# Performance work log

Measured on AMD Instinct MI355X. Metric: run time of the kernel, lower is better.

## Reference

```python
import jax, jax.numpy as jnp
import numpy as np

N = 50000   # nodes
E = 800000  # edges (avg degree 16)
C = 96      # in = hidden = out channels


def setup_inputs() -> dict:
    key = jax.random.key(0)
    ks = jax.random.split(key, 8)
    s = np.float32(1.0 / np.sqrt(C))
    x = jax.random.normal(ks[0], (N, C), dtype=jnp.float32)
    edge_index = jax.random.randint(ks[1], (2, E), 0, N, dtype=jnp.int64)
    W1 = jax.random.normal(ks[2], (C, C), dtype=jnp.float32) * s
    Wr1 = jax.random.normal(ks[3], (C, C), dtype=jnp.float32) * s
    b1 = jnp.zeros((C,), dtype=jnp.float32)
    W2 = jax.random.normal(ks[4], (C, C), dtype=jnp.float32) * s
    Wr2 = jax.random.normal(ks[5], (C, C), dtype=jnp.float32) * s
    b2 = jnp.zeros((C,), dtype=jnp.float32)
    return {"x": x, "edge_index": edge_index,
            "W1": W1, "Wr1": Wr1, "b1": b1,
            "W2": W2, "Wr2": Wr2, "b2": b2}


def spline_conv(x, edge_index, W, W_root, b):
    """Gather-transform-scatter message passing (SplineConv core, mean aggr)."""
    src, dst = edge_index[0], edge_index[1]
    h = x @ W                                   # [N, C] transform once per node
    msg = h[src]                                # [E, C] edge gather
    agg = jax.ops.segment_sum(msg, dst, num_segments=N)        # scatter-add
    deg = jax.ops.segment_sum(jnp.ones((E,), x.dtype), dst, num_segments=N)
    agg = agg / jnp.maximum(deg, 1.0)[:, None]  # mean aggregation
    return agg + x @ W_root + b                 # root weight + bias


def reference(x, edge_index, W1, Wr1, b1, W2, Wr2, b2):
    h = jax.nn.relu(spline_conv(x, edge_index, W1, Wr1, b1))
    out = spline_conv(h, edge_index, W2, Wr2, b2)
    return out.reshape(-1)  # generalization of x.view(1600)
```

## Files before the change

### kernel.cpp

```cpp
#include <hip/hip_runtime.h>

#define C 96
#define BKT_SHIFT 9
#define BKT_SIZE 512
#define CAP 10240
#define EB 2048
typedef unsigned short u16;
typedef unsigned int u32;
typedef __attribute__((ext_vector_type(8))) short short8;
typedef __attribute__((ext_vector_type(4))) float floatx4;

__device__ inline u16 f2bf(float f) {
    union { float f; u32 u; } v; v.f = f;
    u32 r = v.u + 0x7fff + ((v.u >> 16) & 1);
    return (u16)(r >> 16);
}

__global__ __launch_bounds__(256) void prep_kernel(const float* __restrict__ x,
                                                   u16* __restrict__ xb, int n16, int CX,
                                                   const float* W0, const float* W1,
                                                   const float* W2, const float* W3,
                                                   u16* T0, u16* T1, u16* T2, u16* T3,
                                                   int* __restrict__ bkt_cnt) {
    int bid = blockIdx.x;
    int t = threadIdx.x;
    if (bid < CX) {
        int i = bid * 256 + t;
        if (i >= n16) return;
        const float4* p = (const float4*)x + (size_t)i * 4;
        float4 a = p[0], b = p[1], c = p[2], d = p[3];
        short8 o0, o1;
        o0[0] = (short)f2bf(a.x); o0[1] = (short)f2bf(a.y);
        o0[2] = (short)f2bf(a.z); o0[3] = (short)f2bf(a.w);
        o0[4] = (short)f2bf(b.x); o0[5] = (short)f2bf(b.y);
        o0[6] = (short)f2bf(b.z); o0[7] = (short)f2bf(b.w);
        o1[0] = (short)f2bf(c.x); o1[1] = (short)f2bf(c.y);
        o1[2] = (short)f2bf(c.z); o1[3] = (short)f2bf(c.w);
        o1[4] = (short)f2bf(d.x); o1[5] = (short)f2bf(d.y);
        o1[6] = (short)f2bf(d.z); o1[7] = (short)f2bf(d.w);
        *(short8*)(xb + (size_t)i * 16) = o0;
        *(short8*)(xb + (size_t)i * 16 + 8) = o1;
    } else if (bid < CX + 4) {
        int w = bid - CX;
        const float* W = w == 0 ? W0 : w == 1 ? W1 : w == 2 ? W2 : W3;
        u16* T = w == 0 ? T0 : w == 1 ? T1 : w == 2 ? T2 : T3;
        for (int i = t; i < C * C; i += 256) {
            int k = i / C, n = i - k * C;
            T[n * C + k] = f2bf(W[i]);
        }
    } else {
        if (t < 128) bkt_cnt[t] = 0;
    }
}

__global__ __launch_bounds__(256) void binA_kernel(const int* __restrict__ src,
                                                   const int* __restrict__ dst,
                                                   int* __restrict__ bkt_cnt,
                                                   u32* __restrict__ stage, int E) {
    __shared__ u32 s_word[EB];
    __shared__ u32 s_addr[EB];
    __shared__ int s_cnt[128];
    __shared__ int s_inc[128];
    __shared__ int s_base[128];
    int t = threadIdx.x;
    int e0 = blockIdx.x * EB;
    int cnt_here = min(EB, E - e0);

    for (int i = t; i < 128; i += 256) s_cnt[i] = 0;
    __syncthreads();

    int my_src[EB / 256], my_dl[EB / 256], my_b[EB / 256], my_rank[EB / 256];
    int nmine = 0;
#pragma unroll
    for (int k = 0; k < EB / 256; k++) {
        int i = t + k * 256;
        if (i < cnt_here) {
            int s = src[e0 + i], d = dst[e0 + i];
            int b = d >> BKT_SHIFT;
            my_src[nmine] = s;
            my_dl[nmine] = d & (BKT_SIZE - 1);
            my_b[nmine] = b;
            my_rank[nmine] = atomicAdd(&s_cnt[b], 1);
            nmine++;
        }
    }
    __syncthreads();

    if (t < 128) s_inc[t] = s_cnt[t];
    __syncthreads();
    for (int off = 1; off < 128; off <<= 1) {
        int x = (t >= off && t < 128) ? s_inc[t - off] : 0;
        __syncthreads();
        if (t < 128) s_inc[t] += x;
        __syncthreads();
    }

    if (t < 128 && s_cnt[t] > 0)
        s_base[t] = t * CAP + atomicAdd(&bkt_cnt[t], s_cnt[t]);
    __syncthreads();

    for (int k = 0; k < nmine; k++) {
        int b = my_b[k];
        int slot = (s_inc[b] - s_cnt[b]) + my_rank[k];
        s_word[slot] = ((u32)my_dl[k] << 16) | (u32)my_src[k];
        s_addr[slot] = (u32)(s_base[b] + my_rank[k]);
    }
    __syncthreads();

    for (int i = t; i < cnt_here; i += 256) stage[s_addr[i]] = s_word[i];
}

__global__ __launch_bounds__(256) void binB_kernel(const u32* __restrict__ stage,
                                                   const int* __restrict__ bkt_cnt,
                                                   int* __restrict__ deg,
                                                   int* __restrict__ row_off,
                                                   u16* __restrict__ csr, int N) {
    __shared__ int cnt[BKT_SIZE];
    __shared__ int cur[BKT_SIZE];
    __shared__ int ssum[256];
    int b = blockIdx.x;
    int n0 = b << BKT_SHIFT;
    int nn = min(BKT_SIZE, N - n0);
    int t = threadIdx.x;
    int s0 = b * CAP;
    int s1 = s0 + bkt_cnt[b];

    for (int i = t; i < BKT_SIZE; i += 256) cnt[i] = 0;
    __syncthreads();

    for (int i = s0 + t; i < s1; i += 256) atomicAdd(&cnt[stage[i] >> 16], 1);
    __syncthreads();

    int a0 = cnt[2 * t], a1 = cnt[2 * t + 1];
    ssum[t] = a0 + a1;
    __syncthreads();
    for (int off = 1; off < 256; off <<= 1) {
        int x = (t >= off) ? ssum[t - off] : 0;
        __syncthreads();
        ssum[t] += x;
        __syncthreads();
    }
    int excl = ssum[t] - (a0 + a1);
    cur[2 * t] = s0 + excl;
    cur[2 * t + 1] = s0 + excl + a0;
    if (2 * t < nn) { deg[n0 + 2 * t] = a0; row_off[n0 + 2 * t] = s0 + excl; }
    if (2 * t + 1 < nn) { deg[n0 + 2 * t + 1] = a1; row_off[n0 + 2 * t + 1] = s0 + excl + a0; }
    __syncthreads();

    for (int i = s0 + t; i < s1; i += 256) {
        u32 w = stage[i];
        int p = atomicAdd(&cur[w >> 16], 1);
        csr[p] = (u16)(w & 0xffffu);
    }
}

template <bool RELU, typename OT>
__global__ __launch_bounds__(256, 4) void layer_kernel(const u16* __restrict__ X,
                                                       const int* __restrict__ row_off,
                                                       const int* __restrict__ deg,
                                                       const u16* __restrict__ csr,
                                                       const u16* __restrict__ WTA,
                                                       const u16* __restrict__ WTR,
                                                       const float* __restrict__ BIAS,
                                                       OT* __restrict__ Y, int n) {
    __shared__ u16 sA[64 * 104];
    const int t = threadIdx.x;
    const int row0 = blockIdx.x * 64;

    {
        int nl = t >> 2;
        int node = row0 + nl;
        int q = t & 3;
        float acc[24];
#pragma unroll
        for (int i = 0; i < 24; i++) acc[i] = 0.f;
        int d = 0;
        if (node < n) {
            int start = row_off[node];
            d = deg[node];
            const u16* Xq = X + q * 24;
            int j = 0;
            for (; j + 4 <= d; j += 4) {
                int si[4];
#pragma unroll
                for (int k = 0; k < 4; k++) si[k] = csr[start + j + k];
                uint4 v[4][3];
#pragma unroll
                for (int k = 0; k < 4; k++) {
                    const u16* p = Xq + (size_t)si[k] * C;
                    v[k][0] = *(const uint4*)(p);
                    v[k][1] = *(const uint4*)(p + 8);
                    v[k][2] = *(const uint4*)(p + 16);
                }
#pragma unroll
                for (int k = 0; k < 4; k++)
#pragma unroll
                    for (int c = 0; c < 3; c++) {
                        u32 ww[4] = {v[k][c].x, v[k][c].y, v[k][c].z, v[k][c].w};
#pragma unroll
                        for (int i = 0; i < 4; i++) {
                            union { u32 u; float f; } a0, b0;
                            a0.u = ww[i] << 16; b0.u = ww[i] & 0xffff0000u;
                            acc[c * 8 + 2 * i]     += a0.f;
                            acc[c * 8 + 2 * i + 1] += b0.f;
                        }
                    }
            }
            for (; j < d; j++) {
                const u16* p = Xq + (size_t)csr[start + j] * C;
                uint4 v0 = *(const uint4*)(p);
                uint4 v1 = *(const uint4*)(p + 8);
                uint4 v2 = *(const uint4*)(p + 16);
                uint4 vv[3] = {v0, v1, v2};
#pragma unroll
                for (int c = 0; c < 3; c++) {
                    u32 ww[4] = {vv[c].x, vv[c].y, vv[c].z, vv[c].w};
#pragma unroll
                    for (int i = 0; i < 4; i++) {
                        union { u32 u; float f; } a0, b0;
                        a0.u = ww[i] << 16; b0.u = ww[i] & 0xffff0000u;
                        acc[c * 8 + 2 * i]     += a0.f;
                        acc[c * 8 + 2 * i + 1] += b0.f;
                    }
                }
            }
        }
        float inv = 1.0f / fmaxf((float)d, 1.0f);
        u16* dl = sA + nl * 104 + q * 24;
#pragma unroll
        for (int c = 0; c < 3; c++) {
            short8 o;
#pragma unroll
            for (int i = 0; i < 8; i++) o[i] = (short)f2bf(acc[c * 8 + i] * inv);
            *(short8*)(dl + c * 8) = o;
        }
    }
    __syncthreads();

    const int lane = t & 63;
    const int w = t >> 6;
    const int quad = lane >> 4;
    const int l16 = lane & 15;
    const int r0 = row0 + w * 16;

    floatx4 acc6[6];
#pragma unroll
    for (int i = 0; i < 6; i++) acc6[i] = (floatx4){0.f, 0.f, 0.f, 0.f};

    {
        const u16* Ap = sA + (w * 16 + l16) * 104 + quad * 8;
        const u16* Wp = WTA + l16 * C + quad * 8;
#pragma unroll
        for (int ks = 0; ks < 3; ks++) {
            short8 a = *(const short8*)(Ap + ks * 32);
#pragma unroll
            for (int nt = 0; nt < 6; nt++) {
                short8 b = *(const short8*)(Wp + nt * 16 * C + ks * 32);
                acc6[nt] = __builtin_amdgcn_mfma_f32_16x16x32_bf16(a, b, acc6[nt], 0, 0, 0);
            }
        }
    }
    {
        int arow = r0 + l16;
        if (arow >= n) arow = n - 1;
        const u16* Xp = X + (size_t)arow * C + quad * 8;
        const u16* Wp = WTR + l16 * C + quad * 8;
#pragma unroll
        for (int ks = 0; ks < 3; ks++) {
            short8 a = *(const short8*)(Xp + ks * 32);
#pragma unroll
            for (int nt = 0; nt < 6; nt++) {
                short8 b = *(const short8*)(Wp + nt * 16 * C + ks * 32);
                acc6[nt] = __builtin_amdgcn_mfma_f32_16x16x32_bf16(a, b, acc6[nt], 0, 0, 0);
            }
        }
    }

#pragma unroll
    for (int nt = 0; nt < 6; nt++) {
        int cc = nt * 16 + l16;
        float bv = BIAS[cc];
#pragma unroll
        for (int r = 0; r < 4; r++) {
            int row = r0 + quad * 4 + r;
            if (row >= n) continue;
            float v = acc6[nt][r] + bv;
            if (RELU) v = fmaxf(v, 0.f);
            if constexpr (sizeof(OT) == 2) Y[(size_t)row * C + cc] = (OT)f2bf(v);
            else                           Y[(size_t)row * C + cc] = (OT)v;
        }
    }
}

extern "C" void kernel_launch(void* const* d_in, const int* in_sizes, int n_in,
                              void* d_out, int out_size, void* d_ws, size_t ws_size,
                              hipStream_t stream) {
    const float* x   = (const float*)d_in[0];
    const int*   ei  = (const int*)d_in[1];
    const float* W1  = (const float*)d_in[2];
    const float* Wr1 = (const float*)d_in[3];
    const float* b1  = (const float*)d_in[4];
    const float* W2  = (const float*)d_in[5];
    const float* Wr2 = (const float*)d_in[6];
    const float* b2  = (const float*)d_in[7];
    float* out = (float*)d_out;

    const int N = in_sizes[0] / C;
    const int E = in_sizes[1] / 2;
    const int* src = ei;
    const int* dst = ei + E;

    const int nbkt = (N + BKT_SIZE - 1) >> BKT_SHIFT;
    int Npad = (N + 63) & ~63;

    int*   bkt_cnt = (int*)d_ws;
    int*   deg     = bkt_cnt + 128;
    int*   row_off = deg + Npad;
    u32*   stage   = (u32*)(row_off + Npad);
    u16*   csr     = (u16*)(stage + (size_t)nbkt * CAP);
    u16*   xb      = csr + (((size_t)nbkt * CAP + 7) & ~(size_t)7);
    u16*   h1b     = xb + (size_t)N * C;
    u16*   wt      = h1b + (size_t)N * C;
    u16 *wt1 = wt, *wtr1 = wt + C * C, *wt2 = wt + 2 * C * C, *wtr2 = wt + 3 * C * C;

    const int grid64 = (N + 63) / 64;
    const int n16    = N * C / 16;
    const int CX     = (n16 + 255) / 256;
    const int DB     = (E + EB - 1) / EB;

    prep_kernel<<<CX + 5, 256, 0, stream>>>(x, xb, n16, CX,
                                            W1, Wr1, W2, Wr2, wt1, wtr1, wt2, wtr2,
                                            bkt_cnt);
    binA_kernel<<<DB, 256, 0, stream>>>(src, dst, bkt_cnt, stage, E);
    binB_kernel<<<nbkt, 256, 0, stream>>>(stage, bkt_cnt, deg, row_off, csr, N);

    layer_kernel<true, u16><<<grid64, 256, 0, stream>>>(xb, row_off, deg, csr,
                                                        wt1, wtr1, b1, h1b, N);
    layer_kernel<false, float><<<grid64, 256, 0, stream>>>(h1b, row_off, deg, csr,
                                                           wt2, wtr2, b2, out, N);
}
```

Before: 201.6 us.

## Merge prep work into binning kernel and sort rows by degree within blocks

Folds the x-to-bf16 conversion and weight transposition into the edge-binning kernel as extra blocks, leaving a tiny kernel that only zeroes the bucket counters. In the layer kernel, each 64-node block ranks its nodes by degree and assigns them to threads in sorted order, so nodes with similar degree share a wavefront and lanes diverge less in the gather loop. The ranking adds a 64-iteration shared-memory pass and two barriers per block, and the fused kernel's LDS footprint now also applies to the conversion blocks.

```diff
diff --git a/kernel.cpp b/kernel.cpp
--- a/kernel.cpp
+++ b/kernel.cpp
@@ -16,54 +16,56 @@
     return (u16)(r >> 16);
 }
 
-__global__ __launch_bounds__(256) void prep_kernel(const float* __restrict__ x,
+__global__ __launch_bounds__(128) void zero_kernel(int* __restrict__ bkt_cnt) {
+    bkt_cnt[threadIdx.x] = 0;
+}
+
+__global__ __launch_bounds__(256) void binA_kernel(const int* __restrict__ src,
+                                                   const int* __restrict__ dst,
+                                                   int* __restrict__ bkt_cnt,
+                                                   u32* __restrict__ stage, int E, int DB,
+                                                   const float* __restrict__ x,
                                                    u16* __restrict__ xb, int n16, int CX,
                                                    const float* W0, const float* W1,
                                                    const float* W2, const float* W3,
-                                                   u16* T0, u16* T1, u16* T2, u16* T3,
-                                                   int* __restrict__ bkt_cnt) {
+                                                   u16* T0, u16* T1, u16* T2, u16* T3) {
     int bid = blockIdx.x;
     int t = threadIdx.x;
-    if (bid < CX) {
-        int i = bid * 256 + t;
-        if (i >= n16) return;
-        const float4* p = (const float4*)x + (size_t)i * 4;
-        float4 a = p[0], b = p[1], c = p[2], d = p[3];
-        short8 o0, o1;
-        o0[0] = (short)f2bf(a.x); o0[1] = (short)f2bf(a.y);
-        o0[2] = (short)f2bf(a.z); o0[3] = (short)f2bf(a.w);
-        o0[4] = (short)f2bf(b.x); o0[5] = (short)f2bf(b.y);
-        o0[6] = (short)f2bf(b.z); o0[7] = (short)f2bf(b.w);
-        o1[0] = (short)f2bf(c.x); o1[1] = (short)f2bf(c.y);
-        o1[2] = (short)f2bf(c.z); o1[3] = (short)f2bf(c.w);
-        o1[4] = (short)f2bf(d.x); o1[5] = (short)f2bf(d.y);
-        o1[6] = (short)f2bf(d.z); o1[7] = (short)f2bf(d.w);
-        *(short8*)(xb + (size_t)i * 16) = o0;
-        *(short8*)(xb + (size_t)i * 16 + 8) = o1;
-    } else if (bid < CX + 4) {
-        int w = bid - CX;
-        const float* W = w == 0 ? W0 : w == 1 ? W1 : w == 2 ? W2 : W3;
-        u16* T = w == 0 ? T0 : w == 1 ? T1 : w == 2 ? T2 : T3;
-        for (int i = t; i < C * C; i += 256) {
-            int k = i / C, n = i - k * C;
-            T[n * C + k] = f2bf(W[i]);
-        }
-    } else {
-        if (t < 128) bkt_cnt[t] = 0;
-    }
-}
-
-__global__ __launch_bounds__(256) void binA_kernel(const int* __restrict__ src,
-                                                   const int* __restrict__ dst,
-                                                   int* __restrict__ bkt_cnt,
-                                                   u32* __restrict__ stage, int E) {
+    if (bid >= DB) {
+        if (bid < DB + CX) {
+            int i = (bid - DB) * 256 + t;
+            if (i >= n16) return;
+            const float4* p = (const float4*)x + (size_t)i * 4;
+            float4 a = p[0], b = p[1], c = p[2], d = p[3];
+            short8 o0, o1;
+            o0[0] = (short)f2bf(a.x); o0[1] = (short)f2bf(a.y);
+            o0[2] = (short)f2bf(a.z); o0[3] = (short)f2bf(a.w);
+            o0[4] = (short)f2bf(b.x); o0[5] = (short)f2bf(b.y);
+            o0[6] = (short)f2bf(b.z); o0[7] = (short)f2bf(b.w);
+            o1[0] = (short)f2bf(c.x); o1[1] = (short)f2bf(c.y);
+            o1[2] = (short)f2bf(c.z); o1[3] = (short)f2bf(c.w);
+            o1[4] = (short)f2bf(d.x); o1[5] = (short)f2bf(d.y);
+            o1[6] = (short)f2bf(d.z); o1[7] = (short)f2bf(d.w);
+            *(short8*)(xb + (size_t)i * 16) = o0;
+            *(short8*)(xb + (size_t)i * 16 + 8) = o1;
+        } else {
+            int w = bid - DB - CX;
+            const float* W = w == 0 ? W0 : w == 1 ? W1 : w == 2 ? W2 : W3;
+            u16* T = w == 0 ? T0 : w == 1 ? T1 : w == 2 ? T2 : T3;
+            for (int i = t; i < C * C; i += 256) {
+                int k = i / C, n = i - k * C;
+                T[n * C + k] = f2bf(W[i]);
+            }
+        }
+        return;
+    }
+
     __shared__ u32 s_word[EB];
     __shared__ u32 s_addr[EB];
     __shared__ int s_cnt[128];
     __shared__ int s_inc[128];
     __shared__ int s_base[128];
-    int t = threadIdx.x;
-    int e0 = blockIdx.x * EB;
+    int e0 = bid * EB;
     int cnt_here = min(EB, E - e0);
 
     for (int i = t; i < 128; i += 256) s_cnt[i] = 0;
@@ -89,9 +91,9 @@
     if (t < 128) s_inc[t] = s_cnt[t];
     __syncthreads();
     for (int off = 1; off < 128; off <<= 1) {
-        int x = (t >= off && t < 128) ? s_inc[t - off] : 0;
+        int x2 = (t >= off && t < 128) ? s_inc[t - off] : 0;
         __syncthreads();
-        if (t < 128) s_inc[t] += x;
+        if (t < 128) s_inc[t] += x2;
         __syncthreads();
     }
 
@@ -164,11 +166,30 @@
                                                        const float* __restrict__ BIAS,
                                                        OT* __restrict__ Y, int n) {
     __shared__ u16 sA[64 * 104];
+    __shared__ int s_dg[64];
+    __shared__ int s_perm[64];
     const int t = threadIdx.x;
     const int row0 = blockIdx.x * 64;
 
+    if (t < 64) {
+        int node = row0 + t;
+        s_dg[t] = (node < n) ? deg[node] : 0;
+    }
+    __syncthreads();
+    if (t < 64) {
+        int di = s_dg[t];
+        int r = 0;
+#pragma unroll 8
+        for (int j = 0; j < 64; j++) {
+            int dj = s_dg[j];
+            r += (dj < di) || (dj == di && j < t);
+        }
+        s_perm[r] = t;
+    }
+    __syncthreads();
+
     {
-        int nl = t >> 2;
+        int nl = s_perm[t >> 2];
         int node = row0 + nl;
         int q = t & 3;
         float acc[24];
@@ -177,7 +198,7 @@
         int d = 0;
         if (node < n) {
             int start = row_off[node];
-            d = deg[node];
+            d = s_dg[nl];
             const u16* Xq = X + q * 24;
             int j = 0;
             for (; j + 4 <= d; j += 4) {
@@ -208,10 +229,10 @@
             }
             for (; j < d; j++) {
                 const u16* p = Xq + (size_t)csr[start + j] * C;
-                uint4 v0 = *(const uint4*)(p);
-                uint4 v1 = *(const uint4*)(p + 8);
-                uint4 v2 = *(const uint4*)(p + 16);
-                uint4 vv[3] = {v0, v1, v2};
+                uint4 vv[3];
+                vv[0] = *(const uint4*)(p);
+                vv[1] = *(const uint4*)(p + 8);
+                vv[2] = *(const uint4*)(p + 16);
 #pragma unroll
                 for (int c = 0; c < 3; c++) {
                     u32 ww[4] = {vv[c].x, vv[c].y, vv[c].z, vv[c].w};
@@ -328,10 +349,10 @@
     const int CX     = (n16 + 255) / 256;
     const int DB     = (E + EB - 1) / EB;
 
-    prep_kernel<<<CX + 5, 256, 0, stream>>>(x, xb, n16, CX,
-                                            W1, Wr1, W2, Wr2, wt1, wtr1, wt2, wtr2,
-                                            bkt_cnt);
-    binA_kernel<<<DB, 256, 0, stream>>>(src, dst, bkt_cnt, stage, E);
+    zero_kernel<<<1, 128, 0, stream>>>(bkt_cnt);
+    binA_kernel<<<DB + CX + 4, 256, 0, stream>>>(src, dst, bkt_cnt, stage, E, DB,
+                                                 x, xb, n16, CX,
+                                                 W1, Wr1, W2, Wr2, wt1, wtr1, wt2, wtr2);
     binB_kernel<<<nbkt, 256, 0, stream>>>(stage, bkt_cnt, deg, row_off, csr, N);
 
     layer_kernel<true, u16><<<grid64, 256, 0, stream>>>(xb, row_off, deg, csr,
```

Measured after the change: 197.8 us. No clear change (-1.9%).
